# Kernel tuning notes

Measured on AMD Instinct MI355X. Metric: run time of the kernel, lower is better.

The kernel has to match this reference:

```python
import jax, jax.numpy as jnp
import numpy as np

N = 100000   # nodes (rows of origin_data, and unique values in edge_index)
E = 2000000  # edges
CIN = 16     # conv input channels
T = 8        # time dim of origin_data
HUMAN_EXHALATION_FLOW = 0.0001 * 40000  # = 4.0


def setup_inputs() -> dict:
    key = jax.random.key(0)
    k1, k2, k3, k4, k5, k6 = jax.random.split(key, 6)
    # keep size (origin_data[:, -1, 2]) away from zero since it is a divisor
    origin_data = jax.random.uniform(k1, (N, T, 3), jnp.float32) + 0.1
    x = jax.random.normal(k2, (E, 1, CIN), jnp.float32)
    # edge_index must contain every node id 0..N-1 (node_list = zeros_like(edge_index.unique()))
    src = jnp.concatenate([jnp.arange(N, dtype=jnp.int32),
                           jax.random.randint(k3, (E - N,), 0, N, dtype=jnp.int32)])
    dst = jax.random.randint(k4, (E,), 0, N, dtype=jnp.int32)
    edge_index = jnp.stack([src, dst])  # [2, E]
    conv_w = jax.random.normal(k5, (1, CIN, 1, 1), jnp.float32) * 0.1  # [out, in, kh, kw]
    conv_b = jax.random.normal(k6, (1,), jnp.float32) * 0.1
    return {"origin_data": origin_data, "x": x, "conv_w": conv_w,
            "conv_b": conv_b, "edge_index": edge_index}


def reference(origin_data, x, conv_w, conv_b, edge_index):
    concentration = origin_data[:, -1, 0]  # [N]
    people = origin_data[:, -1, 1]         # [N]
    size = origin_data[:, -1, 2]           # [N]

    # 1x1 conv over [1, CIN, E, 1] == per-edge linear: [E,1,CIN] -> [E,1,1]
    out = jnp.einsum('ewc,oc->ewo', x, conv_w[:, :, 0, 0]) + conv_b
    flow = out  # [E,1,1]

    # torch loop uses .item() everywhere -> values are detached constants
    val = jax.lax.stop_gradient(out[:, 0, 0])        # [E]
    conc_d = jax.lax.stop_gradient(concentration)
    size_d = jax.lax.stop_gradient(size)

    src, dst = edge_index[0], edge_index[1]
    valid = src != dst  # self-loops skipped
    # per edge i: write node_list_new[src] = val*conc[src]/size[src] (order 2i)
    #             then node_list_new[dst] = val*conc[src]/size[dst] (order 2i+1)
    v_src = val * conc_d[src] / size_d[src]
    v_dst = val * conc_d[src] / size_d[dst]
    ar = jnp.arange(E, dtype=jnp.int32)
    ids = jnp.concatenate([src, dst])                       # [2E]
    vals = jnp.concatenate([v_src, v_dst])                  # [2E]
    orders = jnp.concatenate([jnp.where(valid, 2 * ar, -1),
                              jnp.where(valid, 2 * ar + 1, -1)])
    max_ord = jax.ops.segment_max(orders, ids, num_segments=N)  # last valid write per node
    sel = (orders >= 0) & (orders == max_ord[ids])              # unique winner per node
    node_list_new = jnp.zeros(N, dtype=val.dtype).at[ids].add(jnp.where(sel, vals, 0.0))

    exhaled = jax.lax.stop_gradient(HUMAN_EXHALATION_FLOW * people / size_d)  # .item() detaches
    result = concentration + node_list_new + exhaled
    return result[:, None], flow
```

## Files before the change

kernel.cpp:

```cpp
#include <hip/hip_runtime.h>

#define N_NODES 100000
#define E_EDGES 2000000
#define SPLIT_E 1800000
#define CIN 16
#define EXH_FLOW 4.0f
#define TOP_E (E_EDGES - SPLIT_E)

#define UNROLL 4
#define ECHUNK (E_EDGES / UNROLL)
#define QTHREADS (E_EDGES * 4 / UNROLL)


__global__ void init_nodes_kernel(const float* __restrict__ origin,
                                  float* __restrict__ out,
                                  int* __restrict__ max_ord,
                                  float* __restrict__ conc_c,
                                  float* __restrict__ rsize_c,
                                  unsigned char* __restrict__ settled) {
    int n = blockIdx.x * blockDim.x + threadIdx.x;
    if (n >= N_NODES) return;
    size_t base = (size_t)n * 24;
    float conc   = origin[base + 21];
    float people = origin[base + 22];
    float size   = origin[base + 23];
    float rs = 1.0f / size;
    out[n] = conc + EXH_FLOW * people * rs;
    conc_c[n]  = conc;
    rsize_c[n] = rs;
    max_ord[n] = -1;
    settled[n] = 0;
}

__global__ void scatter_top_kernel(const int* __restrict__ src,
                                   const int* __restrict__ dst,
                                   int* __restrict__ max_ord,
                                   unsigned char* __restrict__ settled) {
    int i = blockIdx.x * blockDim.x + threadIdx.x;
    int e = SPLIT_E + i;
    if (e >= E_EDGES) return;
    int s = src[e], d = dst[e];
    if (s != d) {
        atomicMax(&max_ord[s], 2 * e);
        atomicMax(&max_ord[d], 2 * e + 1);
        settled[s] = 1;
        settled[d] = 1;
    }
}

__global__ void fused_flow_scatter_kernel(const float4* __restrict__ xv,
                                          const float* __restrict__ w,
                                          const float* __restrict__ b,
                                          const int* __restrict__ src,
                                          const int* __restrict__ dst,
                                          const unsigned char* __restrict__ settled,
                                          float* __restrict__ flow,
                                          int* __restrict__ max_ord) {
    int tid = blockIdx.x * blockDim.x + threadIdx.x;
    if (tid >= QTHREADS) return;
    int q  = tid & 3;
    int e0 = tid >> 2;
    float4 wq = ((const float4*)w)[q];
    float bias = b[0];

    float4 v0 = xv[tid + 0 * QTHREADS];
    float4 v1 = xv[tid + 1 * QTHREADS];
    float4 v2 = xv[tid + 2 * QTHREADS];
    float4 v3 = xv[tid + 3 * QTHREADS];

    float p0 = v0.x * wq.x + v0.y * wq.y + v0.z * wq.z + v0.w * wq.w;
    float p1 = v1.x * wq.x + v1.y * wq.y + v1.z * wq.z + v1.w * wq.w;
    float p2 = v2.x * wq.x + v2.y * wq.y + v2.z * wq.z + v2.w * wq.w;
    float p3 = v3.x * wq.x + v3.y * wq.y + v3.z * wq.z + v3.w * wq.w;

    p0 += __shfl_xor(p0, 1);  p0 += __shfl_xor(p0, 2);
    p1 += __shfl_xor(p1, 1);  p1 += __shfl_xor(p1, 2);
    p2 += __shfl_xor(p2, 1);  p2 += __shfl_xor(p2, 2);
    p3 += __shfl_xor(p3, 1);  p3 += __shfl_xor(p3, 2);

    if (q == 0) {
        int ea = e0, eb = e0 + ECHUNK, ec = e0 + 2 * ECHUNK, ed = e0 + 3 * ECHUNK;
        flow[ea] = p0 + bias;
        flow[eb] = p1 + bias;
        flow[ec] = p2 + bias;
        flow[ed] = p3 + bias;
        int sa = src[ea], da = dst[ea];
        int sb = src[eb], db = dst[eb];
        int sc = src[ec], dc = dst[ec];
        int sd = src[ed], dd = dst[ed];
#define SCAT(EE, SS, DD)                                                  \
        if ((SS) != (DD)) {                                               \
            if (!settled[SS]) atomicMax(&max_ord[SS], 2 * (EE));          \
            if (!settled[DD]) atomicMax(&max_ord[DD], 2 * (EE) + 1);      \
        }
        SCAT(ea, sa, da)
        SCAT(eb, sb, db)
        SCAT(ec, sc, dc)
        SCAT(ed, sd, dd)
#undef SCAT
    }
}

__global__ void finalize_kernel(const int* __restrict__ src,
                                const float* __restrict__ flow,
                                const int* __restrict__ max_ord,
                                const float* __restrict__ conc_c,
                                const float* __restrict__ rsize_c,
                                float* __restrict__ out) {
    int n = blockIdx.x * blockDim.x + threadIdx.x;
    if (n >= N_NODES) return;
    int o = max_ord[n];
    if (o < 0) return;
    int e = o >> 1;
    float val = flow[e];
    float v;
    if ((o & 1) == 0) {
        v = val * conc_c[n] * rsize_c[n];
    } else {
        int s = src[e];
        v = val * conc_c[s] * rsize_c[n];
    }
    out[n] += v;
}

extern "C" void kernel_launch(void* const* d_in, const int* in_sizes, int n_in,
                              void* d_out, int out_size, void* d_ws, size_t ws_size,
                              hipStream_t stream) {
    const float* origin = (const float*)d_in[0];
    const float* x      = (const float*)d_in[1];
    const float* conv_w = (const float*)d_in[2];
    const float* conv_b = (const float*)d_in[3];
    const int*   eidx   = (const int*)d_in[4];
    const int* src = eidx;
    const int* dst = eidx + E_EDGES;

    float* out  = (float*)d_out;
    float* flow = out + N_NODES;

    int*           max_ord = (int*)d_ws;
    float*         conc_c  = (float*)((char*)d_ws + 1 * 400 * 1024);
    float*         rsize_c = (float*)((char*)d_ws + 2 * 400 * 1024);
    unsigned char* settled = (unsigned char*)((char*)d_ws + 3 * 400 * 1024);

    const int BLK = 256;
    init_nodes_kernel<<<(N_NODES + BLK - 1) / BLK, BLK, 0, stream>>>(
        origin, out, max_ord, conc_c, rsize_c, settled);
    scatter_top_kernel<<<(TOP_E + BLK - 1) / BLK, BLK, 0, stream>>>(
        src, dst, max_ord, settled);
    fused_flow_scatter_kernel<<<(QTHREADS + BLK - 1) / BLK, BLK, 0, stream>>>(
        (const float4*)x, conv_w, conv_b, src, dst, settled, flow, max_ord);
    finalize_kernel<<<(N_NODES + BLK - 1) / BLK, BLK, 0, stream>>>(
        src, flow, max_ord, conc_c, rsize_c, out);
}
```

Before: 65.30 us.

## Spread edge scatter across quad lanes and merge node init with top-edge scatter

The main flow kernel now has each of the four quad lanes store one flow value and issue a share of the src/dst atomicMax scatter, where before only lane 0 did all the stores and atomics. The node-init and top-edge scatter kernels are merged into one launch, with the table reset split into a small vectorized init kernel. The aim is to cut per-lane serialization and divergence in the scatter and let node init overlap the top-edge atomics. In exchange, every lane now reloads src/dst for two edges, so index reads are duplicated across the quad.

```diff
diff --git a/kernel.cpp b/kernel.cpp
--- a/kernel.cpp
+++ b/kernel.cpp
@@ -11,40 +11,47 @@
 #define ECHUNK (E_EDGES / UNROLL)
 #define QTHREADS (E_EDGES * 4 / UNROLL)
 
+#define BLK 256
+#define NODE_BLOCKS ((N_NODES + BLK - 1) / BLK)
+#define TOP_BLOCKS  ((TOP_E + BLK - 1) / BLK)
 
-__global__ void init_nodes_kernel(const float* __restrict__ origin,
-                                  float* __restrict__ out,
-                                  int* __restrict__ max_ord,
-                                  float* __restrict__ conc_c,
-                                  float* __restrict__ rsize_c,
-                                  unsigned char* __restrict__ settled) {
-    int n = blockIdx.x * blockDim.x + threadIdx.x;
-    if (n >= N_NODES) return;
-    size_t base = (size_t)n * 24;
-    float conc   = origin[base + 21];
-    float people = origin[base + 22];
-    float size   = origin[base + 23];
-    float rs = 1.0f / size;
-    out[n] = conc + EXH_FLOW * people * rs;
-    conc_c[n]  = conc;
-    rsize_c[n] = rs;
-    max_ord[n] = -1;
-    settled[n] = 0;
+
+__global__ void table_init_kernel(int4* __restrict__ max_ord4,
+                                  uint4* __restrict__ settled4) {
+    int i = blockIdx.x * blockDim.x + threadIdx.x;
+    if (i < N_NODES / 4) max_ord4[i] = make_int4(-1, -1, -1, -1);
+    if (i < N_NODES / 16) settled4[i] = make_uint4(0u, 0u, 0u, 0u);
 }
 
-__global__ void scatter_top_kernel(const int* __restrict__ src,
-                                   const int* __restrict__ dst,
-                                   int* __restrict__ max_ord,
-                                   unsigned char* __restrict__ settled) {
-    int i = blockIdx.x * blockDim.x + threadIdx.x;
-    int e = SPLIT_E + i;
-    if (e >= E_EDGES) return;
-    int s = src[e], d = dst[e];
-    if (s != d) {
-        atomicMax(&max_ord[s], 2 * e);
-        atomicMax(&max_ord[d], 2 * e + 1);
-        settled[s] = 1;
-        settled[d] = 1;
+__global__ void init_and_top_kernel(const float* __restrict__ origin,
+                                    const int* __restrict__ src,
+                                    const int* __restrict__ dst,
+                                    float* __restrict__ out,
+                                    float* __restrict__ conc_c,
+                                    float* __restrict__ rsize_c,
+                                    int* __restrict__ max_ord,
+                                    unsigned char* __restrict__ settled) {
+    if (blockIdx.x < NODE_BLOCKS) {
+        int n = blockIdx.x * BLK + threadIdx.x;
+        if (n >= N_NODES) return;
+        size_t base = (size_t)n * 24;
+        float conc   = origin[base + 21];
+        float people = origin[base + 22];
+        float size   = origin[base + 23];
+        float rs = 1.0f / size;
+        out[n] = conc + EXH_FLOW * people * rs;
+        conc_c[n]  = conc;
+        rsize_c[n] = rs;
+    } else {
+        int e = SPLIT_E + (blockIdx.x - NODE_BLOCKS) * BLK + threadIdx.x;
+        if (e >= E_EDGES) return;
+        int s = src[e], d = dst[e];
+        if (s != d) {
+            atomicMax(&max_ord[s], 2 * e);
+            atomicMax(&max_ord[d], 2 * e + 1);
+            settled[s] = 1;
+            settled[d] = 1;
+        }
     }
 }
 
@@ -78,26 +85,22 @@
     p2 += __shfl_xor(p2, 1);  p2 += __shfl_xor(p2, 2);
     p3 += __shfl_xor(p3, 1);  p3 += __shfl_xor(p3, 2);
 
-    if (q == 0) {
-        int ea = e0, eb = e0 + ECHUNK, ec = e0 + 2 * ECHUNK, ed = e0 + 3 * ECHUNK;
-        flow[ea] = p0 + bias;
-        flow[eb] = p1 + bias;
-        flow[ec] = p2 + bias;
-        flow[ed] = p3 + bias;
-        int sa = src[ea], da = dst[ea];
-        int sb = src[eb], db = dst[eb];
-        int sc = src[ec], dc = dst[ec];
-        int sd = src[ed], dd = dst[ed];
-#define SCAT(EE, SS, DD)                                                  \
-        if ((SS) != (DD)) {                                               \
-            if (!settled[SS]) atomicMax(&max_ord[SS], 2 * (EE));          \
-            if (!settled[DD]) atomicMax(&max_ord[DD], 2 * (EE) + 1);      \
-        }
-        SCAT(ea, sa, da)
-        SCAT(eb, sb, db)
-        SCAT(ec, sc, dc)
-        SCAT(ed, sd, dd)
-#undef SCAT
+    float pq = (q == 0) ? p0 : ((q == 1) ? p1 : ((q == 2) ? p2 : p3));
+    flow[e0 + q * ECHUNK] = pq + bias;
+
+    int side = q >> 1;
+    int c1 = (q & 1), c2 = (q & 1) + 2;
+    int ea = e0 + c1 * ECHUNK;
+    int eb = e0 + c2 * ECHUNK;
+    int sa = src[ea], da = dst[ea];
+    int sb = src[eb], db = dst[eb];
+    if (sa != da) {
+        int idx = side ? da : sa;
+        if (!settled[idx]) atomicMax(&max_ord[idx], 2 * ea + side);
+    }
+    if (sb != db) {
+        int idx = side ? db : sb;
+        if (!settled[idx]) atomicMax(&max_ord[idx], 2 * eb + side);
     }
 }
 
@@ -142,11 +145,10 @@
     float*         rsize_c = (float*)((char*)d_ws + 2 * 400 * 1024);
     unsigned char* settled = (unsigned char*)((char*)d_ws + 3 * 400 * 1024);
 
-    const int BLK = 256;
-    init_nodes_kernel<<<(N_NODES + BLK - 1) / BLK, BLK, 0, stream>>>(
-        origin, out, max_ord, conc_c, rsize_c, settled);
-    scatter_top_kernel<<<(TOP_E + BLK - 1) / BLK, BLK, 0, stream>>>(
-        src, dst, max_ord, settled);
+    table_init_kernel<<<(N_NODES / 4 + BLK - 1) / BLK, BLK, 0, stream>>>(
+        (int4*)max_ord, (uint4*)settled);
+    init_and_top_kernel<<<NODE_BLOCKS + TOP_BLOCKS, BLK, 0, stream>>>(
+        origin, src, dst, out, conc_c, rsize_c, max_ord, settled);
     fused_flow_scatter_kernel<<<(QTHREADS + BLK - 1) / BLK, BLK, 0, stream>>>(
         (const float4*)x, conv_w, conv_b, src, dst, settled, flow, max_ord);
     finalize_kernel<<<(N_NODES + BLK - 1) / BLK, BLK, 0, stream>>>(
```

Measured after the change: 64.64 us, median of 2. No clear change (-1.0%).
